# Performance work log

Hardware: AMD Instinct MI355X
Metric: run time of the kernel (lower is better)

The kernel has to match this reference:

```python
import jax, jax.numpy as jnp
import numpy as np

IN_F, OUT_F = 256, 256
GRID, ORDER = 5, 3
K = GRID + ORDER + 1  # 9 knots
EPS_MINMAX = 1e-7     # K.epsilon()
EPS_BN = 1e-3         # keras BatchNormalization default epsilon


def setup_inputs() -> dict:
    key = jax.random.key(0)
    ks = jax.random.split(key, 4)
    x = jax.random.normal(ks[0], (32, 32, 32, IN_F), dtype=jnp.float32)
    he = lambda k, shape, fan_in: jax.random.normal(k, shape, jnp.float32) * np.sqrt(2.0 / fan_in)
    base_weight = he(ks[1], (IN_F, OUT_F), IN_F)
    spline_weight = he(ks[2], (OUT_F, IN_F, K), IN_F * K)
    spline_scaler = jnp.ones((OUT_F, IN_F), jnp.float32)
    return {
        'x': x,
        'base_weight': base_weight,
        'spline_weight': spline_weight,
        'spline_scaler': spline_scaler,
        'bn_base_gamma': jnp.ones((OUT_F,), jnp.float32),
        'bn_base_beta': jnp.zeros((OUT_F,), jnp.float32),
        'bn_base_mean': jnp.zeros((OUT_F,), jnp.float32),
        'bn_base_var': jnp.ones((OUT_F,), jnp.float32),
        'bn_spline_gamma': jnp.ones((OUT_F,), jnp.float32),
        'bn_spline_beta': jnp.zeros((OUT_F,), jnp.float32),
        'bn_spline_mean': jnp.zeros((OUT_F,), jnp.float32),
        'bn_spline_var': jnp.ones((OUT_F,), jnp.float32),
    }


def _bn(z, gamma, beta, mean, var):
    # Keras BatchNormalization, inference mode (training=False)
    return gamma * (z - mean) * jax.lax.rsqrt(var + EPS_BN) + beta


def reference(x, base_weight, spline_weight, spline_scaler,
              bn_base_gamma, bn_base_beta, bn_base_mean, bn_base_var,
              bn_spline_gamma, bn_spline_beta, bn_spline_mean, bn_spline_var):
    B, H, W, _ = x.shape
    xf = x.reshape(-1, IN_F)  # [N, in]

    # base path: GEMM -> BN -> SiLU
    base = xf @ base_weight
    base = jax.nn.silu(_bn(base, bn_base_gamma, bn_base_beta, bn_base_mean, bn_base_var))

    # min-max normalize per feature over the flattened batch
    x_min = jnp.min(xf, axis=0, keepdims=True)
    x_max = jnp.max(xf, axis=0, keepdims=True)
    xn = (xf - x_min) / (x_max - x_min + EPS_MINMAX)

    # triangle basis: relu(1 - |x - knot|), knots = linspace(-1, 1, K)
    knots = jnp.linspace(-1.0, 1.0, K, dtype=jnp.float32)
    basis = jnp.maximum(0.0, 1.0 - jnp.abs(xn[:, :, None] - knots[None, None, :]))  # [N, in, K]

    # scaled spline weight, flattened GEMM
    w = (spline_weight * spline_scaler[:, :, None]).reshape(OUT_F, IN_F * K)  # [out, in*K]
    spline = basis.reshape(-1, IN_F * K) @ w.T  # [N, out]
    spline = _bn(spline, bn_spline_gamma, bn_spline_beta, bn_spline_mean, bn_spline_var)

    out = base + spline
    return out.reshape(B, H, W, OUT_F)
```

## Files before the change

### kernel.cpp

```cpp
#include <hip/hip_runtime.h>
#include <stdint.h>
#include <stddef.h>

typedef _Float16 h2 __attribute__((ext_vector_type(2)));
typedef _Float16 h8 __attribute__((ext_vector_type(8)));
typedef float f4 __attribute__((ext_vector_type(4)));

union Hfrag { h2 p[4]; h8 v; };

#define WS_PMIN   0
#define WS_PMAX   524288
#define WS_BT     0
#define WS_SMALL  1048576
#define WS_SCALEV (WS_SMALL + 0)
#define WS_BKN    (WS_SMALL + 1024)
#define WS_C0     (WS_SMALL + 3072)
#define WS_BSC    (WS_SMALL + 4096)
#define WS_BSH    (WS_SMALL + 5120)
#define WS_SSC    (WS_SMALL + 6144)
#define WS_SSH    (WS_SMALL + 7168)

__global__ __launch_bounds__(256) void kan_minmax(const float* __restrict__ x,
                                                  float* __restrict__ pmin,
                                                  float* __restrict__ pmax) {
  __shared__ f4 smn[4][64], smx[4][64];
  const int b = blockIdx.x, t = threadIdx.x;
  const int fq = t & 63, rg = t >> 6;
  const float* p = x + (size_t)b * 64 * 256 + (size_t)rg * 16 * 256 + fq * 4;
  f4 mn = (f4)(3.402823466e38f), mx = (f4)(-3.402823466e38f);
#pragma unroll
  for (int j = 0; j < 16; ++j) {
    f4 v = *(const f4*)(p + (size_t)j * 256);
    mn = __builtin_elementwise_min(mn, v);
    mx = __builtin_elementwise_max(mx, v);
  }
  smn[rg][fq] = mn; smx[rg][fq] = mx;
  __syncthreads();
  if (rg == 0) {
#pragma unroll
    for (int g = 1; g < 4; ++g) {
      mn = __builtin_elementwise_min(mn, smn[g][fq]);
      mx = __builtin_elementwise_max(mx, smx[g][fq]);
    }
    *(f4*)(pmin + (size_t)b * 256 + fq * 4) = mn;
    *(f4*)(pmax + (size_t)b * 256 + fq * 4) = mx;
  }
}

__global__ __launch_bounds__(256) void kan_finalize(
    const float* __restrict__ pmin, const float* __restrict__ pmax,
    const float* __restrict__ g1, const float* __restrict__ b1,
    const float* __restrict__ m1, const float* __restrict__ v1,
    const float* __restrict__ g2, const float* __restrict__ b2,
    const float* __restrict__ m2, const float* __restrict__ v2,
    float* __restrict__ scalev, _Float16* __restrict__ bkn,
    float* __restrict__ bscv, float* __restrict__ bshv,
    float* __restrict__ sscv, float* __restrict__ sshv) {
  __shared__ f4 smn[256], smx[256];
  const int t = threadIdx.x, q = blockIdx.x;
  const float* pm = pmin + (size_t)t * 256 + q * 4;
  const float* px = pmax + (size_t)t * 256 + q * 4;
  f4 mn = __builtin_elementwise_min(*(const f4*)pm, *(const f4*)(pm + 256 * 256));
  f4 mx = __builtin_elementwise_max(*(const f4*)px, *(const f4*)(px + 256 * 256));
  smn[t] = mn; smx[t] = mx;
  __syncthreads();
  for (int st = 128; st > 0; st >>= 1) {
    if (t < st) {
      smn[t] = __builtin_elementwise_min(smn[t], smn[t + st]);
      smx[t] = __builtin_elementwise_max(smx[t], smx[t + st]);
    }
    __syncthreads();
  }
  if (t == 0) {
    const f4 fmn = smn[0], fmx = smx[0];
#pragma unroll
    for (int j = 0; j < 4; ++j) {
      const int o = q * 4 + j;
      const float mnS = fmn[j], mxS = fmx[j];
      const float rng = mxS - mnS + 1e-7f;
      scalev[o] = 1.0f / rng;
      const float step = 0.25f * rng;
#pragma unroll
      for (int jj = 0; jj < 4; ++jj)
        bkn[jj * 256 + o] = (_Float16)(mnS + step * (float)jj);
      const float bs = g1[o] / sqrtf(v1[o] + 1e-3f);
      bscv[o] = bs;
      bshv[o] = b1[o] - m1[o] * bs;
      const float ss = g2[o] / sqrtf(v2[o] + 1e-3f);
      sscv[o] = ss;
      sshv[o] = b2[o] - m2[o] * ss;
    }
  }
}

__global__ __launch_bounds__(256) void kan_buildw(
    const float* __restrict__ spline_w, const float* __restrict__ spline_s,
    const float* __restrict__ base_w, const float* __restrict__ scalev,
    _Float16* __restrict__ Bt, float* __restrict__ C0) {
  const int og = blockIdx.x;
  const int i  = threadIdx.x;
  const float* wp = spline_w + (size_t)(og * 256 + i) * 9;
  const float w1 = wp[1], w2 = wp[2], w3 = wp[3], w4 = wp[4];
  const float w5 = wp[5], w6 = wp[6], w7 = wp[7], w8 = wp[8];
  const float s  = spline_s[og * 256 + i];
  const float sc = scalev[i];
  const float wp0 = 0.25f*w1 + 0.5f*w2 + 0.75f*w3 + w4 + 0.75f*w5 + 0.5f*w6 + 0.25f*w7;
  float wj[4];
  wj[0] = (w5 + w6 + w7 + w8) - (w1 + w2 + w3 + w4);
  wj[1] = w1 - 2.0f * w5;
  wj[2] = w2 - 2.0f * w6;
  wj[3] = w3 - 2.0f * w7;
  const float ssc = s * sc;
  const int half = og >> 7, o = og & 127, ic = i >> 5, kk = i & 31;
#pragma unroll
  for (int j = 0; j < 4; ++j) {
    const int ks = j * 8 + ic;
    Bt[((size_t)(ks * 2 + half) * 128 + o) * 32 + kk] = (_Float16)(wj[j] * ssc);
  }
  Bt[((size_t)((32 + ic) * 2 + half) * 128 + o) * 32 + kk] =
      (_Float16)base_w[(size_t)i * 256 + og];
  __shared__ float red[256];
  red[i] = wp0 * s;
  __syncthreads();
  for (int st = 128; st > 0; st >>= 1) {
    if (i < st) red[i] += red[i + st];
    __syncthreads();
  }
  if (i == 0) C0[og] = red[0];
}

__global__ __launch_bounds__(256, 2) void kan_gemm(
    const float* __restrict__ x, const _Float16* __restrict__ Bt,
    const _Float16* __restrict__ bkn, const float* __restrict__ C0,
    const float* __restrict__ bscv, const float* __restrict__ bshv,
    const float* __restrict__ sscv, const float* __restrict__ sshv,
    float* __restrict__ out) {
  const int tid = threadIdx.x;
  const int lane = tid & 63;
  const int wv = tid >> 6;
  const int wm = wv >> 1, wn = wv & 1;
  const int lr = lane & 15, lg = lane >> 4;
  const int mt = blockIdx.x & 255, nt = blockIdx.x >> 8;

  const int rowA = mt * 128 + wm * 64 + lr;
  const int colB = wn * 64 + lr;

  f4 accS[4][4], accB[4][4];
#pragma unroll
  for (int m = 0; m < 4; ++m)
#pragma unroll
    for (int n = 0; n < 4; ++n) { accS[m][n] = (f4)0.0f; accB[m][n] = (f4)0.0f; }

  const char* btbase = (const char*)Bt + (size_t)nt * 8192 + (size_t)colB * 64 + (size_t)lg * 16;

  h2 hz; hz[0] = (_Float16)0.0f; hz[1] = (_Float16)0.0f;

  f4 xa[4], xb[4];
  {
    const int ib = lg * 8;
#pragma unroll
    for (int m = 0; m < 4; ++m) {
      const float* px = x + (size_t)(rowA + m * 16) * 256 + ib;
      xa[m] = *(const f4*)px; xb[m] = *(const f4*)(px + 4);
    }
  }

#define SPLINE_STEP(J, BF)                                                   \
  {                                                                          \
    Hfrag bbj;                                                               \
    bbj.v = *(const h8*)(bkn + (J) * 256 + ic * 32 + lg * 8);                \
    _Pragma("unroll")                                                        \
    for (int m = 0; m < 4; ++m) {                                            \
      Hfrag afm;                                                             \
      _Pragma("unroll")                                                      \
      for (int qq = 0; qq < 4; ++qq) {                                       \
        h2 d = xh[m].p[qq] - bbj.p[qq];                                      \
        afm.p[qq] = __builtin_elementwise_max(d, hz);                        \
      }                                                                      \
      _Pragma("unroll")                                                      \
      for (int n = 0; n < 4; ++n)                                            \
        accS[m][n] = __builtin_amdgcn_mfma_f32_16x16x32_f16(afm.v, BF[n].v,  \
                                                            accS[m][n], 0, 0, 0); \
    }                                                                        \
  }

#define LOADB(BF, BYTEOFF)                                                   \
  _Pragma("unroll")                                                          \
  for (int n = 0; n < 4; ++n)                                                \
    BF[n].v = *(const h8*)(bpic + (BYTEOFF) + n * 1024);

#pragma unroll 1
  for (int ic = 0; ic < 8; ++ic) {
    const char* bpic = btbase + (size_t)ic * 16384;

    Hfrag bfA[4], bfB[4];
    LOADB(bfA, 0)

    Hfrag xh[4];
#pragma unroll
    for (int m = 0; m < 4; ++m) {
      xh[m].p[0][0] = (_Float16)xa[m].x; xh[m].p[0][1] = (_Float16)xa[m].y;
      xh[m].p[1][0] = (_Float16)xa[m].z; xh[m].p[1][1] = (_Float16)xa[m].w;
      xh[m].p[2][0] = (_Float16)xb[m].x; xh[m].p[2][1] = (_Float16)xb[m].y;
      xh[m].p[3][0] = (_Float16)xb[m].z; xh[m].p[3][1] = (_Float16)xb[m].w;
    }

    LOADB(bfB, 131072)
    SPLINE_STEP(0, bfA)
    LOADB(bfA, 262144)
    SPLINE_STEP(1, bfB)
    LOADB(bfB, 393216)
    SPLINE_STEP(2, bfA)
    LOADB(bfA, 524288)
    SPLINE_STEP(3, bfB)

#pragma unroll
    for (int m = 0; m < 4; ++m)
#pragma unroll
      for (int n = 0; n < 4; ++n)
        accB[m][n] = __builtin_amdgcn_mfma_f32_16x16x32_f16(xh[m].v, bfA[n].v, accB[m][n], 0, 0, 0);

    __builtin_amdgcn_sched_barrier(0);
    if (ic < 7) {
      const int ib = (ic + 1) * 32 + lg * 8;
#pragma unroll
      for (int m = 0; m < 4; ++m) {
        const float* px = x + (size_t)(rowA + m * 16) * 256 + ib;
        xa[m] = *(const f4*)px; xb[m] = *(const f4*)(px + 4);
      }
    }
  }
#undef SPLINE_STEP
#undef LOADB

#pragma unroll
  for (int n = 0; n < 4; ++n) {
    const int col = nt * 128 + colB + n * 16;
    const float vbs = bscv[col], vbh = bshv[col];
    const float vss = sscv[col];
    const float vsh = sshv[col] + vss * C0[col];
#pragma unroll
    for (int m = 0; m < 4; ++m) {
      const int row0 = mt * 128 + wm * 64 + m * 16 + lg * 4;
#pragma unroll
      for (int r = 0; r < 4; ++r) {
        const float zb = accB[m][n][r] * vbs + vbh;
        const float si = zb / (1.0f + __expf(-zb));
        const float val = si + accS[m][n][r] * vss + vsh;
        out[(size_t)(row0 + r) * 256 + col] = val;
      }
    }
  }
}

extern "C" void kernel_launch(void* const* d_in, const int* in_sizes, int n_in,
                              void* d_out, int out_size, void* d_ws, size_t ws_size,
                              hipStream_t stream) {
  const float* x        = (const float*)d_in[0];
  const float* base_w   = (const float*)d_in[1];
  const float* spline_w = (const float*)d_in[2];
  const float* spline_s = (const float*)d_in[3];
  const float* g1 = (const float*)d_in[4];
  const float* b1 = (const float*)d_in[5];
  const float* m1 = (const float*)d_in[6];
  const float* v1 = (const float*)d_in[7];
  const float* g2 = (const float*)d_in[8];
  const float* b2 = (const float*)d_in[9];
  const float* m2 = (const float*)d_in[10];
  const float* v2 = (const float*)d_in[11];
  float* out = (float*)d_out;
  char* ws = (char*)d_ws;

  float* pmin     = (float*)(ws + WS_PMIN);
  float* pmax     = (float*)(ws + WS_PMAX);
  _Float16* Bt    = (_Float16*)(ws + WS_BT);
  float* scalev   = (float*)(ws + WS_SCALEV);
  _Float16* bkn   = (_Float16*)(ws + WS_BKN);
  float* C0       = (float*)(ws + WS_C0);
  float* bscv     = (float*)(ws + WS_BSC);
  float* bshv     = (float*)(ws + WS_BSH);
  float* sscv     = (float*)(ws + WS_SSC);
  float* sshv     = (float*)(ws + WS_SSH);

  kan_minmax<<<512, 256, 0, stream>>>(x, pmin, pmax);
  kan_finalize<<<64, 256, 0, stream>>>(pmin, pmax, g1, b1, m1, v1, g2, b2, m2, v2,
                                       scalev, bkn, bscv, bshv, sscv, sshv);
  kan_buildw<<<256, 256, 0, stream>>>(spline_w, spline_s, base_w, scalev, Bt, C0);
  kan_gemm<<<512, 256, 0, stream>>>(x, Bt, bkn, C0, bscv, bshv, sscv, sshv, out);
}
```

Baseline: 151.2 us.

## Stage B weight tiles in LDS via global_load_lds with padded layout

The weight-prep kernel now writes B in a padded layout with an 80-byte row stride. In the GEMM, each K-chunk of B for the block's N-tile is copied straight into shared memory with global_load_lds, and the MFMA fragments then read from LDS instead of global memory. The knot table is also kept in LDS. This shares B loads across the four waves and lets the padding cut bank conflicts, at the cost of a barrier and a full vmcnt wait before each chunk with no double buffering, and about 52KB of LDS per block, which may limit occupancy.

```diff
diff --git a/kernel.cpp b/kernel.cpp
--- a/kernel.cpp
+++ b/kernel.cpp
@@ -19,6 +19,12 @@
 #define WS_BSH    (WS_SMALL + 5120)
 #define WS_SSC    (WS_SMALL + 6144)
 #define WS_SSH    (WS_SMALL + 7168)
+
+__device__ __forceinline__ void gload_lds16(const void* g, void* l) {
+  __builtin_amdgcn_global_load_lds(
+      (const __attribute__((address_space(1))) void*)g,
+      (__attribute__((address_space(3))) void*)l, 16, 0, 0);
+}
 
 __global__ __launch_bounds__(256) void kan_minmax(const float* __restrict__ x,
                                                   float* __restrict__ pmin,
@@ -112,13 +118,11 @@
   wj[3] = w3 - 2.0f * w7;
   const float ssc = s * sc;
   const int half = og >> 7, o = og & 127, ic = i >> 5, kk = i & 31;
-#pragma unroll
-  for (int j = 0; j < 4; ++j) {
-    const int ks = j * 8 + ic;
-    Bt[((size_t)(ks * 2 + half) * 128 + o) * 32 + kk] = (_Float16)(wj[j] * ssc);
-  }
-  Bt[((size_t)((32 + ic) * 2 + half) * 128 + o) * 32 + kk] =
-      (_Float16)base_w[(size_t)i * 256 + og];
+  const size_t base = (size_t)ic * 64000 + (size_t)half * 25600 + (size_t)o * 40 + kk;
+#pragma unroll
+  for (int j = 0; j < 4; ++j)
+    Bt[base + (size_t)j * 5120] = (_Float16)(wj[j] * ssc);
+  Bt[base + 4 * 5120] = (_Float16)base_w[(size_t)i * 256 + og];
   __shared__ float red[256];
   red[i] = wp0 * s;
   __syncthreads();
@@ -145,15 +149,19 @@
   const int rowA = mt * 128 + wm * 64 + lr;
   const int colB = wn * 64 + lr;
 
+  __shared__ __align__(16) char smem[53248];
+  _Float16* sbkn = (_Float16*)(smem + 51200);
+  *(uint2*)(sbkn + tid * 4) = ((const uint2*)bkn)[tid];
+
   f4 accS[4][4], accB[4][4];
 #pragma unroll
   for (int m = 0; m < 4; ++m)
 #pragma unroll
     for (int n = 0; n < 4; ++n) { accS[m][n] = (f4)0.0f; accB[m][n] = (f4)0.0f; }
 
-  const char* btbase = (const char*)Bt + (size_t)nt * 8192 + (size_t)colB * 64 + (size_t)lg * 16;
-
   h2 hz; hz[0] = (_Float16)0.0f; hz[1] = (_Float16)0.0f;
+
+  const int rowb = colB * 80 + lg * 16;
 
   f4 xa[4], xb[4];
   {
@@ -165,10 +173,15 @@
     }
   }
 
+#define LOADB(BF, J)                                                         \
+  _Pragma("unroll")                                                          \
+  for (int n = 0; n < 4; ++n)                                                \
+    BF[n].v = *(const h8*)(smem + rowb + (J) * 10240 + n * 1280);
+
 #define SPLINE_STEP(J, BF)                                                   \
   {                                                                          \
     Hfrag bbj;                                                               \
-    bbj.v = *(const h8*)(bkn + (J) * 256 + ic * 32 + lg * 8);                \
+    bbj.v = *(const h8*)(sbkn + (J) * 256 + ic * 32 + lg * 8);               \
     _Pragma("unroll")                                                        \
     for (int m = 0; m < 4; ++m) {                                            \
       Hfrag afm;                                                             \
@@ -184,17 +197,20 @@
     }                                                                        \
   }
 
-#define LOADB(BF, BYTEOFF)                                                   \
-  _Pragma("unroll")                                                          \
-  for (int n = 0; n < 4; ++n)                                                \
-    BF[n].v = *(const h8*)(bpic + (BYTEOFF) + n * 1024);
-
 #pragma unroll 1
   for (int ic = 0; ic < 8; ++ic) {
-    const char* bpic = btbase + (size_t)ic * 16384;
-
-    Hfrag bfA[4], bfB[4];
-    LOADB(bfA, 0)
+    __syncthreads();
+    {
+      const char* gsrc = (const char*)Bt + (size_t)ic * 128000 + (size_t)nt * 51200;
+#pragma unroll
+      for (int r = 0; r < 13; ++r) {
+        const int idx = r * 256 + tid;
+        if (idx < 3200)
+          gload_lds16(gsrc + (size_t)idx * 16, smem + r * 4096 + wv * 1024);
+      }
+    }
+    asm volatile("s_waitcnt vmcnt(0)" ::: "memory");
+    __syncthreads();
 
     Hfrag xh[4];
 #pragma unroll
@@ -205,21 +221,6 @@
       xh[m].p[3][0] = (_Float16)xb[m].z; xh[m].p[3][1] = (_Float16)xb[m].w;
     }
 
-    LOADB(bfB, 131072)
-    SPLINE_STEP(0, bfA)
-    LOADB(bfA, 262144)
-    SPLINE_STEP(1, bfB)
-    LOADB(bfB, 393216)
-    SPLINE_STEP(2, bfA)
-    LOADB(bfA, 524288)
-    SPLINE_STEP(3, bfB)
-
-#pragma unroll
-    for (int m = 0; m < 4; ++m)
-#pragma unroll
-      for (int n = 0; n < 4; ++n)
-        accB[m][n] = __builtin_amdgcn_mfma_f32_16x16x32_f16(xh[m].v, bfA[n].v, accB[m][n], 0, 0, 0);
-
     __builtin_amdgcn_sched_barrier(0);
     if (ic < 7) {
       const int ib = (ic + 1) * 32 + lg * 8;
@@ -229,6 +230,24 @@
         xa[m] = *(const f4*)px; xb[m] = *(const f4*)(px + 4);
       }
     }
+    __builtin_amdgcn_sched_barrier(0);
+
+    Hfrag bfA[4], bfB[4];
+    LOADB(bfA, 0)
+    LOADB(bfB, 1)
+    SPLINE_STEP(0, bfA)
+    LOADB(bfA, 2)
+    SPLINE_STEP(1, bfB)
+    LOADB(bfB, 3)
+    SPLINE_STEP(2, bfA)
+    LOADB(bfA, 4)
+    SPLINE_STEP(3, bfB)
+
+#pragma unroll
+    for (int m = 0; m < 4; ++m)
+#pragma unroll
+      for (int n = 0; n < 4; ++n)
+        accB[m][n] = __builtin_amdgcn_mfma_f32_16x16x32_f16(xh[m].v, bfA[n].v, accB[m][n], 0, 0, 0);
   }
 #undef SPLINE_STEP
 #undef LOADB
```

Result: faster. 143.6 us (-5.0%).

## Stage B weight tiles into LDS via async global-to-LDS loads with ring buffer

Applied to the files above, without the earlier changes.

The GEMM kernel now streams the packed fp16 weight tiles into a six-slot LDS ring buffer with global_load_lds and explicit vmcnt waits and barriers, instead of each wave loading B fragments straight from global memory. The prep kernel writes Bt in a padded 40-half row layout so LDS reads avoid bank conflicts, and the knot table is cached in LDS. MFMA blocks run under raised s_setprio. The aim is to share B across waves and overlap its loads with compute, at the cost of about 74KB of LDS per block, which may cut occupancy, plus fragile hand-written waitcnt counts.

```diff
diff --git a/kernel.cpp b/kernel.cpp
--- a/kernel.cpp
+++ b/kernel.cpp
@@ -19,6 +19,12 @@
 #define WS_BSH    (WS_SMALL + 5120)
 #define WS_SSC    (WS_SMALL + 6144)
 #define WS_SSH    (WS_SMALL + 7168)
+
+__device__ __forceinline__ void gload_lds16(const void* g, void* l) {
+  __builtin_amdgcn_global_load_lds(
+      (const __attribute__((address_space(1))) void*)g,
+      (__attribute__((address_space(3))) void*)l, 16, 0, 0);
+}
 
 __global__ __launch_bounds__(256) void kan_minmax(const float* __restrict__ x,
                                                   float* __restrict__ pmin,
@@ -112,13 +118,12 @@
   wj[3] = w3 - 2.0f * w7;
   const float ssc = s * sc;
   const int half = og >> 7, o = og & 127, ic = i >> 5, kk = i & 31;
-#pragma unroll
-  for (int j = 0; j < 4; ++j) {
-    const int ks = j * 8 + ic;
-    Bt[((size_t)(ks * 2 + half) * 128 + o) * 32 + kk] = (_Float16)(wj[j] * ssc);
-  }
-  Bt[((size_t)((32 + ic) * 2 + half) * 128 + o) * 32 + kk] =
-      (_Float16)base_w[(size_t)i * 256 + og];
+  const size_t sec0 = (size_t)(ic * 2 + half) * 5;
+  const size_t off = (size_t)o * 40 + kk;
+#pragma unroll
+  for (int j = 0; j < 4; ++j)
+    Bt[(sec0 + j) * 6144 + off] = (_Float16)(wj[j] * ssc);
+  Bt[(sec0 + 4) * 6144 + off] = (_Float16)base_w[(size_t)i * 256 + og];
   __shared__ float red[256];
   red[i] = wp0 * s;
   __syncthreads();
@@ -145,93 +150,183 @@
   const int rowA = mt * 128 + wm * 64 + lr;
   const int colB = wn * 64 + lr;
 
+  __shared__ __align__(16) char smem[75776];
+  _Float16* sbkn = (_Float16*)(smem + 73728);
+  *(uint2*)((char*)sbkn + tid * 8) = ((const uint2*)bkn)[tid];
+
   f4 accS[4][4], accB[4][4];
 #pragma unroll
   for (int m = 0; m < 4; ++m)
 #pragma unroll
     for (int n = 0; n < 4; ++n) { accS[m][n] = (f4)0.0f; accB[m][n] = (f4)0.0f; }
 
-  const char* btbase = (const char*)Bt + (size_t)nt * 8192 + (size_t)colB * 64 + (size_t)lg * 16;
-
   h2 hz; hz[0] = (_Float16)0.0f; hz[1] = (_Float16)0.0f;
 
-  f4 xa[4], xb[4];
-  {
-    const int ib = lg * 8;
-#pragma unroll
-    for (int m = 0; m < 4; ++m) {
-      const float* px = x + (size_t)(rowA + m * 16) * 256 + ib;
-      xa[m] = *(const f4*)px; xb[m] = *(const f4*)(px + 4);
-    }
-  }
-
-#define SPLINE_STEP(J, BF)                                                   \
+  const int rowb = colB * 80 + lg * 16;
+
+#define STAGE(ICP, J, SLOT)                                                  \
+  {                                                                          \
+    const char* gs = (const char*)Bt + (size_t)((((ICP) * 2 + nt) * 5) + (J)) * 12288; \
+    _Pragma("unroll")                                                        \
+    for (int r = 0; r < 3; ++r)                                              \
+      gload_lds16(gs + (size_t)(r * 256 + tid) * 16,                         \
+                  smem + (SLOT) * 12288 + r * 4096 + wv * 1024);             \
+  }
+
+#define LOADB(BF, SLOT)                                                      \
+  _Pragma("unroll")                                                          \
+  for (int n = 0; n < 4; ++n)                                                \
+    BF[n].v = *(const h8*)(smem + (SLOT) * 12288 + rowb + n * 1280);
+
+#define SPLINE_STEP(J, BF, IC)                                               \
   {                                                                          \
     Hfrag bbj;                                                               \
-    bbj.v = *(const h8*)(bkn + (J) * 256 + ic * 32 + lg * 8);                \
-    _Pragma("unroll")                                                        \
-    for (int m = 0; m < 4; ++m) {                                            \
-      Hfrag afm;                                                             \
+    bbj.v = *(const h8*)(sbkn + (J) * 256 + (IC) * 32 + lg * 8);             \
+    Hfrag af[4];                                                             \
+    _Pragma("unroll")                                                        \
+    for (int m = 0; m < 4; ++m)                                              \
       _Pragma("unroll")                                                      \
       for (int qq = 0; qq < 4; ++qq) {                                       \
         h2 d = xh[m].p[qq] - bbj.p[qq];                                      \
-        afm.p[qq] = __builtin_elementwise_max(d, hz);                        \
+        af[m].p[qq] = __builtin_elementwise_max(d, hz);                      \
       }                                                                      \
+    __builtin_amdgcn_s_setprio(1);                                           \
+    _Pragma("unroll")                                                        \
+    for (int m = 0; m < 4; ++m)                                              \
       _Pragma("unroll")                                                      \
       for (int n = 0; n < 4; ++n)                                            \
-        accS[m][n] = __builtin_amdgcn_mfma_f32_16x16x32_f16(afm.v, BF[n].v,  \
+        accS[m][n] = __builtin_amdgcn_mfma_f32_16x16x32_f16(af[m].v, BF[n].v,\
                                                             accS[m][n], 0, 0, 0); \
+    __builtin_amdgcn_s_setprio(0);                                           \
+  }
+
+#define BASE_STEP(BF)                                                        \
+  {                                                                          \
+    __builtin_amdgcn_s_setprio(1);                                           \
+    _Pragma("unroll")                                                        \
+    for (int m = 0; m < 4; ++m)                                              \
+      _Pragma("unroll")                                                      \
+      for (int n = 0; n < 4; ++n)                                            \
+        accB[m][n] = __builtin_amdgcn_mfma_f32_16x16x32_f16(xh[m].v, BF[n].v,\
+                                                            accB[m][n], 0, 0, 0); \
+    __builtin_amdgcn_s_setprio(0);                                           \
+  }
+
+#define CVT_XH()                                                             \
+  _Pragma("unroll")                                                          \
+  for (int m = 0; m < 4; ++m) {                                              \
+    xh[m].p[0][0] = (_Float16)xa[m].x; xh[m].p[0][1] = (_Float16)xa[m].y;    \
+    xh[m].p[1][0] = (_Float16)xa[m].z; xh[m].p[1][1] = (_Float16)xa[m].w;    \
+    xh[m].p[2][0] = (_Float16)xb[m].x; xh[m].p[2][1] = (_Float16)xb[m].y;    \
+    xh[m].p[3][0] = (_Float16)xb[m].z; xh[m].p[3][1] = (_Float16)xb[m].w;    \
+  }
+
+#define LOAD_X(IC)                                                           \
+  {                                                                          \
+    const int ib = (IC) * 32 + lg * 8;                                       \
+    _Pragma("unroll")                                                        \
+    for (int m = 0; m < 4; ++m) {                                            \
+      const float* px = x + (size_t)(rowA + m * 16) * 256 + ib;              \
+      xa[m] = *(const f4*)px; xb[m] = *(const f4*)(px + 4);                  \
     }                                                                        \
   }
 
-#define LOADB(BF, BYTEOFF)                                                   \
-  _Pragma("unroll")                                                          \
-  for (int n = 0; n < 4; ++n)                                                \
-    BF[n].v = *(const h8*)(bpic + (BYTEOFF) + n * 1024);
-
+  f4 xa[4], xb[4];
+  Hfrag xh[4];
+  LOAD_X(0)
+#pragma unroll
+  for (int j = 0; j < 5; ++j) STAGE(0, j, j)
+  asm volatile("s_waitcnt lgkmcnt(0)" ::: "memory");
+
+  int base = 0;
 #pragma unroll 1
-  for (int ic = 0; ic < 8; ++ic) {
-    const char* bpic = btbase + (size_t)ic * 16384;
-
-    Hfrag bfA[4], bfB[4];
-    LOADB(bfA, 0)
-
-    Hfrag xh[4];
-#pragma unroll
-    for (int m = 0; m < 4; ++m) {
-      xh[m].p[0][0] = (_Float16)xa[m].x; xh[m].p[0][1] = (_Float16)xa[m].y;
-      xh[m].p[1][0] = (_Float16)xa[m].z; xh[m].p[1][1] = (_Float16)xa[m].w;
-      xh[m].p[2][0] = (_Float16)xb[m].x; xh[m].p[2][1] = (_Float16)xb[m].y;
-      xh[m].p[3][0] = (_Float16)xb[m].z; xh[m].p[3][1] = (_Float16)xb[m].w;
-    }
-
-    LOADB(bfB, 131072)
-    SPLINE_STEP(0, bfA)
-    LOADB(bfA, 262144)
-    SPLINE_STEP(1, bfB)
-    LOADB(bfB, 393216)
-    SPLINE_STEP(2, bfA)
-    LOADB(bfA, 524288)
-    SPLINE_STEP(3, bfB)
-
-#pragma unroll
-    for (int m = 0; m < 4; ++m)
-#pragma unroll
-      for (int n = 0; n < 4; ++n)
-        accB[m][n] = __builtin_amdgcn_mfma_f32_16x16x32_f16(xh[m].v, bfA[n].v, accB[m][n], 0, 0, 0);
-
-    __builtin_amdgcn_sched_barrier(0);
-    if (ic < 7) {
-      const int ib = (ic + 1) * 32 + lg * 8;
-#pragma unroll
-      for (int m = 0; m < 4; ++m) {
-        const float* px = x + (size_t)(rowA + m * 16) * 256 + ib;
-        xa[m] = *(const f4*)px; xb[m] = *(const f4*)(px + 4);
-      }
-    }
+  for (int ic = 0; ic < 7; ++ic) {
+    int rs0 = base;
+    int rs1 = rs0 + 1; if (rs1 >= 6) rs1 -= 6;
+    int rs2 = rs1 + 1; if (rs2 >= 6) rs2 -= 6;
+    int rs3 = rs2 + 1; if (rs3 >= 6) rs3 -= 6;
+    int rs4 = rs3 + 1; if (rs4 >= 6) rs4 -= 6;
+    const int ws0 = rs0 ? rs0 - 1 : 5;
+
+    Hfrag b0[4], b1[4];
+
+    __builtin_amdgcn_s_barrier();
+    __builtin_amdgcn_sched_barrier(0);
+    STAGE(ic + 1, 0, ws0)
+    __builtin_amdgcn_sched_barrier(0);
+    asm volatile("s_waitcnt vmcnt(12)" ::: "memory");
+    __builtin_amdgcn_sched_barrier(0);
+    LOADB(b0, rs0)
+    LOADB(b1, rs1)
+    CVT_XH()
+    LOAD_X(ic + 1)
+    SPLINE_STEP(0, b0, ic)
+
+    __builtin_amdgcn_s_barrier();
+    __builtin_amdgcn_sched_barrier(0);
+    STAGE(ic + 1, 1, rs0)
+    __builtin_amdgcn_sched_barrier(0);
+    asm volatile("s_waitcnt vmcnt(20)" ::: "memory");
+    __builtin_amdgcn_sched_barrier(0);
+    LOADB(b0, rs2)
+    SPLINE_STEP(1, b1, ic)
+
+    __builtin_amdgcn_s_barrier();
+    __builtin_amdgcn_sched_barrier(0);
+    STAGE(ic + 1, 2, rs1)
+    __builtin_amdgcn_sched_barrier(0);
+    asm volatile("s_waitcnt vmcnt(20)" ::: "memory");
+    __builtin_amdgcn_sched_barrier(0);
+    LOADB(b1, rs3)
+    SPLINE_STEP(2, b0, ic)
+
+    __builtin_amdgcn_s_barrier();
+    __builtin_amdgcn_sched_barrier(0);
+    STAGE(ic + 1, 3, rs2)
+    __builtin_amdgcn_sched_barrier(0);
+    asm volatile("s_waitcnt vmcnt(20)" ::: "memory");
+    __builtin_amdgcn_sched_barrier(0);
+    LOADB(b0, rs4)
+    SPLINE_STEP(3, b1, ic)
+
+    __builtin_amdgcn_s_barrier();
+    __builtin_amdgcn_sched_barrier(0);
+    STAGE(ic + 1, 4, rs3)
+    __builtin_amdgcn_sched_barrier(0);
+    BASE_STEP(b0)
+
+    base = base ? base - 1 : 5;
+  }
+
+  {
+    __builtin_amdgcn_s_barrier();
+    __builtin_amdgcn_sched_barrier(0);
+    asm volatile("s_waitcnt vmcnt(0)" ::: "memory");
+    __builtin_amdgcn_sched_barrier(0);
+    int rs0 = base;
+    int rs1 = rs0 + 1; if (rs1 >= 6) rs1 -= 6;
+    int rs2 = rs1 + 1; if (rs2 >= 6) rs2 -= 6;
+    int rs3 = rs2 + 1; if (rs3 >= 6) rs3 -= 6;
+    int rs4 = rs3 + 1; if (rs4 >= 6) rs4 -= 6;
+    Hfrag b0[4], b1[4];
+    CVT_XH()
+    LOADB(b0, rs0)
+    LOADB(b1, rs1)
+    SPLINE_STEP(0, b0, 7)
+    LOADB(b0, rs2)
+    SPLINE_STEP(1, b1, 7)
+    LOADB(b1, rs3)
+    SPLINE_STEP(2, b0, 7)
+    LOADB(b0, rs4)
+    SPLINE_STEP(3, b1, 7)
+    BASE_STEP(b0)
   }
 #undef SPLINE_STEP
+#undef BASE_STEP
 #undef LOADB
+#undef STAGE
+#undef CVT_XH
+#undef LOAD_X
 
 #pragma unroll
   for (int n = 0; n < 4; ++n) {
```

Result: faster. 144.4 us (-4.4%).
